# Optimization experiments

Measured on AMD Instinct MI355X. Metric: run time of the kernel, lower is better.

Reference implementation:

```python
import jax, jax.numpy as jnp
import numpy as np

IN_FEATURES = 4096
OUT_FEATURES = 768
N_BITS = 8
SCALE = float(2 ** N_BITS - 1)  # 255
REG_WEIGHT = 0.001


def setup_inputs() -> dict:
    key = jax.random.key(0)
    k1, k2, k3 = jax.random.split(key, 3)
    latent = jax.random.normal(k1, (1024, IN_FEATURES), dtype=jnp.float32)
    true_sum = jax.random.uniform(k2, (1024, OUT_FEATURES * N_BITS), dtype=jnp.float32)
    # nn.init.uniform_(weight, -0.1, 0.1)
    weight = jax.random.uniform(k3, (IN_FEATURES, OUT_FEATURES * N_BITS),
                                dtype=jnp.float32, minval=-0.1, maxval=0.1)
    return {"latent": latent, "true_sum": true_sum, "weight": weight}


def _powers():
    # [1, 2, 4, ..., 2^(n-1)] with the top (sign) bit negated -> two's complement
    p = 2.0 ** jnp.arange(N_BITS, dtype=jnp.float32)
    return p.at[-1].multiply(-1.0)


def reference(latent, true_sum, weight):
    prob_weights = jax.nn.sigmoid(weight)                      # [in, out*n_bits]
    # min(|p-0|, |p-1|) = min(p, 1-p) for p in (0,1)
    reg_loss = REG_WEIGHT * jnp.minimum(prob_weights, 1.0 - prob_weights).mean()

    powers = _powers()                                         # [n_bits]
    int_weights = jnp.einsum('iob,b->io',
                             prob_weights.reshape(IN_FEATURES, -1, N_BITS),
                             powers)                           # [in, out]
    int_sum = jnp.einsum('nob,b->no',
                         true_sum.reshape(true_sum.shape[0], -1, N_BITS),
                         powers)                               # [B, out]

    # (latent[:, :, None] * int_weights[None]).sum(-2) == latent @ int_weights
    pred = jnp.einsum('bi,io->bo', latent, int_weights)        # [B, out]

    recon_loss = jnp.mean((pred / SCALE - int_sum / SCALE) ** 2)
    return (recon_loss + reg_loss, recon_loss, reg_loss)
```

## Files before the change

### kernel.cpp

```cpp
#include <hip/hip_runtime.h>
#include <hip/hip_bf16.h>
#include <stdint.h>

#define IN_F   4096
#define OUT_F  768
#define OUTB   (OUT_F * 8)
#define BATCH  1024
#define SPLITK 4
#define KSPAN  (IN_F / SPLITK)
#define BK     64
#define NIT    (KSPAN / BK)
#define PLANE  (BATCH * OUT_F)
#define PLANE4 (PLANE / 4)
#define EPIBLK 768

#define WS_WP    12582912
#define WS_LABF  18874368
#define WS_REGP  27262976
#define WS_SQP   27269120

typedef short short8  __attribute__((ext_vector_type(8)));
typedef float f32x4   __attribute__((ext_vector_type(4)));
typedef unsigned int u32;

__device__ __forceinline__ ushort f2bf(float f) {
    uint32_t u = __builtin_bit_cast(uint32_t, f);
    u += 0x7FFFu + ((u >> 16) & 1u);
    return (ushort)(u >> 16);
}

__device__ __forceinline__ float waveReduceSum(float v) {
    #pragma unroll
    for (int off = 32; off > 0; off >>= 1) v += __shfl_down(v, off, 64);
    return v;
}

__device__ __forceinline__ void glds16(const void* g, void* l) {
    __builtin_amdgcn_global_load_lds(
        (const __attribute__((address_space(1))) u32*)g,
        (__attribute__((address_space(3))) u32*)l, 16, 0, 0);
}

__global__ __launch_bounds__(256) void k_weights(const float* __restrict__ w,
                                                 const float* __restrict__ latent,
                                                 ushort* __restrict__ wp,
                                                 ushort* __restrict__ labf,
                                                 float* __restrict__ regpart) {
    if (blockIdx.x >= 1536) {
        int t = (blockIdx.x - 1536) * 256 + threadIdx.x;
        const float4* src = (const float4*)latent;
        uint4* dst = (uint4*)labf;
        #pragma unroll
        for (int j = 0; j < 4; j++) {
            int o = j * 131072 + t;
            float4 a0 = src[2 * o];
            float4 a1 = src[2 * o + 1];
            union { ushort u[8]; uint4 v; } pk;
            pk.u[0] = f2bf(a0.x); pk.u[1] = f2bf(a0.y); pk.u[2] = f2bf(a0.z); pk.u[3] = f2bf(a0.w);
            pk.u[4] = f2bf(a1.x); pk.u[5] = f2bf(a1.y); pk.u[6] = f2bf(a1.z); pk.u[7] = f2bf(a1.w);
            dst[o] = pk.v;
        }
        return;
    }

    int t  = blockIdx.x * 256 + threadIdx.x;
    int o  = t % OUT_F;
    int i8 = t / OUT_F;
    const float* src = w + (size_t)(i8 * 8) * OUTB + (size_t)o * 8;

    const float P[8] = {1.f, 2.f, 4.f, 8.f, 16.f, 32.f, 64.f, -128.f};
    float regsum = 0.f;
    union { ushort u[8]; uint4 v; } pk;

    #pragma unroll
    for (int r = 0; r < 8; r++) {
        float4 a = *(const float4*)(src + (size_t)r * OUTB);
        float4 b = *(const float4*)(src + (size_t)r * OUTB + 4);
        float x[8] = {a.x, a.y, a.z, a.w, b.x, b.y, b.z, b.w};
        float iw = 0.f;
        #pragma unroll
        for (int j = 0; j < 8; j++) {
            float p = __builtin_amdgcn_rcpf(1.f + __expf(-x[j]));
            iw += p * P[j];
            regsum += fminf(p, 1.f - p);
        }
        pk.u[r] = f2bf(iw);
    }
    *(uint4*)(wp + ((size_t)i8 * OUT_F + o) * 8) = pk.v;

    float ws = waveReduceSum(regsum);
    __shared__ float red[4];
    int lane = threadIdx.x & 63, wv = threadIdx.x >> 6;
    if (lane == 0) red[wv] = ws;
    __syncthreads();
    if (threadIdx.x == 0) regpart[blockIdx.x] = red[0] + red[1] + red[2] + red[3];
}

__global__ __launch_bounds__(256) void k_gemm(const ushort* __restrict__ labf,
                                              const ushort* __restrict__ wp,
                                              float* __restrict__ predp) {
    __shared__ __align__(16) ushort lA3[3][64 * 64];
    __shared__ __align__(16) ushort lB3[3][8 * 512];

    const int tid  = threadIdx.x;
    const int n0   = blockIdx.x * 64;
    const int m0   = blockIdx.y * 64;
    const int bz   = blockIdx.z;
    const int kbase = bz * KSPAN;
    const int kg0   = kbase >> 3;
    const int lane = tid & 63, w = tid >> 6;
    const int wm = w >> 1, wn = w & 1;
    const int quad = lane >> 4, l16 = lane & 15;
    const int xA = (l16 & 7) << 4;

    f32x4 acc[2][2] = {{{0.f,0.f,0.f,0.f},{0.f,0.f,0.f,0.f}},
                       {{0.f,0.f,0.f,0.f},{0.f,0.f,0.f,0.f}}};

    const int r8 = lane >> 3;
    const int c8 = (lane & 7) ^ r8;
    const int p0 = 2 * w, p1 = 2 * w + 1;
    const ushort* aSrc0 = labf + (size_t)(m0 + 8 * p0 + r8) * IN_F + kbase + 8 * c8;
    const ushort* aSrc1 = labf + (size_t)(m0 + 8 * p1 + r8) * IN_F + kbase + 8 * c8;
    const ushort* bSrc0 = wp + ((size_t)(kg0 + p0) * OUT_F + n0 + lane) * 8;
    const ushort* bSrc1 = wp + ((size_t)(kg0 + p1) * OUT_F + n0 + lane) * 8;

    #define STAGE(bi, it_) do {                                                   \
        glds16(aSrc0 + (size_t)(it_) * BK,              &lA3[bi][p0 * 512]);      \
        glds16(aSrc1 + (size_t)(it_) * BK,              &lA3[bi][p1 * 512]);      \
        glds16(bSrc0 + (size_t)(it_) * (8 * OUT_F * 8), &lB3[bi][p0 * 512]);      \
        glds16(bSrc1 + (size_t)(it_) * (8 * OUT_F * 8), &lB3[bi][p1 * 512]);      \
    } while (0)

    #define MSTEP(bi) do {                                                        \
        const char* Ab = (const char*)&lA3[bi][0];                                \
        _Pragma("unroll")                                                         \
        for (int ss = 0; ss < 2; ++ss) {                                          \
            short8 af0 = *(const short8*)(Ab + ((wm * 32 + l16) << 7)             \
                                             + ((ss * 64 + quad * 16) ^ xA));     \
            short8 af1 = *(const short8*)(Ab + ((wm * 32 + 16 + l16) << 7)        \
                                             + ((ss * 64 + quad * 16) ^ xA));     \
            short8 bf0 = *(const short8*)&lB3[bi][(ss * 4 + quad) * 512           \
                                                  + (wn * 32 + l16) * 8];         \
            short8 bf1 = *(const short8*)&lB3[bi][(ss * 4 + quad) * 512           \
                                                  + (wn * 32 + 16 + l16) * 8];    \
            acc[0][0] = __builtin_amdgcn_mfma_f32_16x16x32_bf16(af0, bf0, acc[0][0], 0, 0, 0); \
            acc[0][1] = __builtin_amdgcn_mfma_f32_16x16x32_bf16(af0, bf1, acc[0][1], 0, 0, 0); \
            acc[1][0] = __builtin_amdgcn_mfma_f32_16x16x32_bf16(af1, bf0, acc[1][0], 0, 0, 0); \
            acc[1][1] = __builtin_amdgcn_mfma_f32_16x16x32_bf16(af1, bf1, acc[1][1], 0, 0, 0); \
        }                                                                         \
    } while (0)

    STAGE(0, 0);
    STAGE(1, 1);
    asm volatile("s_waitcnt vmcnt(4)" ::: "memory");
    __builtin_amdgcn_s_barrier();
    __builtin_amdgcn_sched_barrier(0);

    int bR = 0, bW = 2;
    for (int it = 0; it < NIT - 2; ++it) {
        STAGE(bW, it + 2);
        MSTEP(bR);
        asm volatile("s_waitcnt vmcnt(4)" ::: "memory");
        __builtin_amdgcn_s_barrier();
        __builtin_amdgcn_sched_barrier(0);
        bR = (bR + 1 == 3) ? 0 : bR + 1;
        bW = (bW + 1 == 3) ? 0 : bW + 1;
    }
    MSTEP(bR);
    asm volatile("s_waitcnt vmcnt(0)" ::: "memory");
    __builtin_amdgcn_s_barrier();
    __builtin_amdgcn_sched_barrier(0);
    bR = (bR + 1 == 3) ? 0 : bR + 1;
    MSTEP(bR);

    #undef STAGE
    #undef MSTEP

    float* plane = predp + (size_t)bz * PLANE;
    #pragma unroll
    for (int fm = 0; fm < 2; fm++)
    #pragma unroll
    for (int fn = 0; fn < 2; fn++)
    #pragma unroll
    for (int r = 0; r < 4; r++) {
        int m = m0 + wm * 32 + fm * 16 + quad * 4 + r;
        int n = n0 + wn * 32 + fn * 16 + l16;
        plane[(size_t)m * OUT_F + n] = acc[fm][fn][r];
    }
}

__global__ __launch_bounds__(256) void k_epi(const float* __restrict__ predp,
                                             const float* __restrict__ tsum,
                                             float* __restrict__ sqpart) {
    int g = blockIdx.x * 256 + threadIdx.x;
    int m = g / (OUT_F / 4);
    int c = g % (OUT_F / 4);
    const float4* pp = (const float4*)predp;
    float4 p0 = pp[g];
    float4 p1 = pp[g + PLANE4];
    float4 p2 = pp[g + 2 * PLANE4];
    float4 p3 = pp[g + 3 * PLANE4];
    float pv[4] = {p0.x + p1.x + p2.x + p3.x, p0.y + p1.y + p2.y + p3.y,
                   p0.z + p1.z + p2.z + p3.z, p0.w + p1.w + p2.w + p3.w};
    const float* ts = tsum + (size_t)m * OUTB + (size_t)c * 32;
    float lsum = 0.f;
    #pragma unroll
    for (int j = 0; j < 4; j++) {
        float4 t0 = *(const float4*)(ts + j * 8);
        float4 t1 = *(const float4*)(ts + j * 8 + 4);
        float isum = t0.x + 2.f * t0.y + 4.f * t0.z + 8.f * t0.w
                   + 16.f * t1.x + 32.f * t1.y + 64.f * t1.z - 128.f * t1.w;
        float d = pv[j] - isum;
        lsum += d * d;
    }
    float wsum = waveReduceSum(lsum);
    __shared__ float red[4];
    if ((threadIdx.x & 63) == 0) red[threadIdx.x >> 6] = wsum;
    __syncthreads();
    if (threadIdx.x == 0)
        sqpart[blockIdx.x] = red[0] + red[1] + red[2] + red[3];
}

__global__ __launch_bounds__(256) void k_fin(const float* __restrict__ regpart,
                                             const float* __restrict__ sqpart,
                                             float* __restrict__ out) {
    int tid = threadIdx.x;
    float r = 0.f, s = 0.f;
    #pragma unroll
    for (int j = 0; j < 6; j++) r += regpart[tid + j * 256];
    #pragma unroll
    for (int j = 0; j < 3; j++) s += sqpart[tid + j * 256];
    r = waveReduceSum(r);
    s = waveReduceSum(s);
    __shared__ float redR[4], redS[4];
    int lane = tid & 63, wv = tid >> 6;
    if (lane == 0) { redR[wv] = r; redS[wv] = s; }
    __syncthreads();
    if (tid == 0) {
        float R = redR[0] + redR[1] + redR[2] + redR[3];
        float S = redS[0] + redS[1] + redS[2] + redS[3];
        float recon = S / ((float)(BATCH * OUT_F) * 255.f * 255.f);
        float reg   = 0.001f * R / (float)((size_t)IN_F * OUTB);
        out[0] = recon + reg;
        out[1] = recon;
        out[2] = reg;
    }
}

extern "C" void kernel_launch(void* const* d_in, const int* in_sizes, int n_in,
                              void* d_out, int out_size, void* d_ws, size_t ws_size,
                              hipStream_t stream) {
    const float* latent = (const float*)d_in[0];
    const float* tsum   = (const float*)d_in[1];
    const float* weight = (const float*)d_in[2];
    float* out      = (float*)d_out;
    float* predp    = (float*)d_ws;
    ushort* wp      = (ushort*)((char*)d_ws + WS_WP);
    ushort* labf    = (ushort*)((char*)d_ws + WS_LABF);
    float* regpart  = (float*)((char*)d_ws + WS_REGP);
    float* sqpart   = (float*)((char*)d_ws + WS_SQP);

    k_weights<<<2048, 256, 0, stream>>>(weight, latent, wp, labf, regpart);
    k_gemm<<<dim3(OUT_F / 64, BATCH / 64, SPLITK), 256, 0, stream>>>(labf, wp, predp);
    k_epi<<<EPIBLK, 256, 0, stream>>>(predp, tsum, sqpart);
    k_fin<<<1, 256, 0, stream>>>(regpart, sqpart, out);
}
```

Measured before the change: 199.0 us.

## Enlarge GEMM tile to 128x192 with specialized loader waves and split-K 8

Rebuilds the GEMM around a 128x192 output tile per 384-thread block. Each wave now computes a 64x64 sub-tile with 16 MFMA accumulators, so more compute is done per byte loaded from LDS and global memory. Two waves load the A tile and four load the B tile, each waiting on its own outstanding-load count. The K step drops to 32 and split-K doubles to 8 to keep enough blocks in flight. The cost is that the partial-sum planes written and re-read by the epilogue double in size, and the workspace grows to match.

```diff
diff --git a/kernel.cpp b/kernel.cpp
--- a/kernel.cpp
+++ b/kernel.cpp
@@ -6,18 +6,20 @@
 #define OUT_F  768
 #define OUTB   (OUT_F * 8)
 #define BATCH  1024
-#define SPLITK 4
+#define SPLITK 8
 #define KSPAN  (IN_F / SPLITK)
-#define BK     64
-#define NIT    (KSPAN / BK)
+#define KSTEP  32
+#define NIT    (KSPAN / KSTEP)
+#define TN     192
+#define TM     128
 #define PLANE  (BATCH * OUT_F)
 #define PLANE4 (PLANE / 4)
 #define EPIBLK 768
 
-#define WS_WP    12582912
-#define WS_LABF  18874368
-#define WS_REGP  27262976
-#define WS_SQP   27269120
+#define WS_WP    25165824
+#define WS_LABF  31457280
+#define WS_REGP  39845888
+#define WS_SQP   39852032
 
 typedef short short8  __attribute__((ext_vector_type(8)));
 typedef float f32x4   __attribute__((ext_vector_type(4)));
@@ -96,63 +98,71 @@
     if (threadIdx.x == 0) regpart[blockIdx.x] = red[0] + red[1] + red[2] + red[3];
 }
 
-__global__ __launch_bounds__(256) void k_gemm(const ushort* __restrict__ labf,
+__global__ __launch_bounds__(384) void k_gemm(const ushort* __restrict__ labf,
                                               const ushort* __restrict__ wp,
                                               float* __restrict__ predp) {
-    __shared__ __align__(16) ushort lA3[3][64 * 64];
-    __shared__ __align__(16) ushort lB3[3][8 * 512];
+    __shared__ __align__(16) ushort lA[3][8 * 512];
+    __shared__ __align__(16) ushort lB[3][12 * 512];
 
     const int tid  = threadIdx.x;
-    const int n0   = blockIdx.x * 64;
-    const int m0   = blockIdx.y * 64;
+    const int lane = tid & 63, w = tid >> 6;
+    const int n0   = blockIdx.x * TN;
+    const int m0   = blockIdx.y * TM;
     const int bz   = blockIdx.z;
     const int kbase = bz * KSPAN;
     const int kg0   = kbase >> 3;
-    const int lane = tid & 63, w = tid >> 6;
-    const int wm = w >> 1, wn = w & 1;
     const int quad = lane >> 4, l16 = lane & 15;
-    const int xA = (l16 & 7) << 4;
-
-    f32x4 acc[2][2] = {{{0.f,0.f,0.f,0.f},{0.f,0.f,0.f,0.f}},
-                       {{0.f,0.f,0.f,0.f},{0.f,0.f,0.f,0.f}}};
-
-    const int r8 = lane >> 3;
-    const int c8 = (lane & 7) ^ r8;
-    const int p0 = 2 * w, p1 = 2 * w + 1;
-    const ushort* aSrc0 = labf + (size_t)(m0 + 8 * p0 + r8) * IN_F + kbase + 8 * c8;
-    const ushort* aSrc1 = labf + (size_t)(m0 + 8 * p1 + r8) * IN_F + kbase + 8 * c8;
-    const ushort* bSrc0 = wp + ((size_t)(kg0 + p0) * OUT_F + n0 + lane) * 8;
-    const ushort* bSrc1 = wp + ((size_t)(kg0 + p1) * OUT_F + n0 + lane) * 8;
-
-    #define STAGE(bi, it_) do {                                                   \
-        glds16(aSrc0 + (size_t)(it_) * BK,              &lA3[bi][p0 * 512]);      \
-        glds16(aSrc1 + (size_t)(it_) * BK,              &lA3[bi][p1 * 512]);      \
-        glds16(bSrc0 + (size_t)(it_) * (8 * OUT_F * 8), &lB3[bi][p0 * 512]);      \
-        glds16(bSrc1 + (size_t)(it_) * (8 * OUT_F * 8), &lB3[bi][p1 * 512]);      \
+    const int wmh = w & 1;
+    const int wnt = w >> 1;
+
+    f32x4 acc[4][4] = {};
+
+    const int r4 = lane >> 2, c4 = lane & 3;
+    const int kgw = w - 2;
+
+    #define STAGE(bi, it_) do {                                                        \
+        if (w < 2) {                                                                   \
+            _Pragma("unroll")                                                          \
+            for (int k = 0; k < 4; ++k) {                                              \
+                int p = 4 * w + k;                                                     \
+                glds16(labf + (size_t)(m0 + 16 * p + r4) * IN_F                        \
+                            + kbase + (it_) * KSTEP + c4 * 8,                          \
+                       &lA[bi][p * 512]);                                              \
+            }                                                                          \
+        } else {                                                                       \
+            _Pragma("unroll")                                                          \
+            for (int h = 0; h < 3; ++h) {                                              \
+                glds16(wp + ((size_t)(kg0 + (it_) * 4 + kgw) * OUT_F                   \
+                             + n0 + h * 64 + lane) * 8,                                \
+                       &lB[bi][(kgw * 3 + h) * 512]);                                  \
+            }                                                                          \
+        }                                                                              \
     } while (0)
 
-    #define MSTEP(bi) do {                                                        \
-        const char* Ab = (const char*)&lA3[bi][0];                                \
-        _Pragma("unroll")                                                         \
-        for (int ss = 0; ss < 2; ++ss) {                                          \
-            short8 af0 = *(const short8*)(Ab + ((wm * 32 + l16) << 7)             \
-                                             + ((ss * 64 + quad * 16) ^ xA));     \
-            short8 af1 = *(const short8*)(Ab + ((wm * 32 + 16 + l16) << 7)        \
-                                             + ((ss * 64 + quad * 16) ^ xA));     \
-            short8 bf0 = *(const short8*)&lB3[bi][(ss * 4 + quad) * 512           \
-                                                  + (wn * 32 + l16) * 8];         \
-            short8 bf1 = *(const short8*)&lB3[bi][(ss * 4 + quad) * 512           \
-                                                  + (wn * 32 + 16 + l16) * 8];    \
-            acc[0][0] = __builtin_amdgcn_mfma_f32_16x16x32_bf16(af0, bf0, acc[0][0], 0, 0, 0); \
-            acc[0][1] = __builtin_amdgcn_mfma_f32_16x16x32_bf16(af0, bf1, acc[0][1], 0, 0, 0); \
-            acc[1][0] = __builtin_amdgcn_mfma_f32_16x16x32_bf16(af1, bf0, acc[1][0], 0, 0, 0); \
-            acc[1][1] = __builtin_amdgcn_mfma_f32_16x16x32_bf16(af1, bf1, acc[1][1], 0, 0, 0); \
-        }                                                                         \
+    #define WAITOWN() do {                                                             \
+        if (w < 2) asm volatile("s_waitcnt vmcnt(4)" ::: "memory");                    \
+        else       asm volatile("s_waitcnt vmcnt(3)" ::: "memory");                    \
+    } while (0)
+
+    #define MSTEP(bi) do {                                                             \
+        short8 af[4], bf[4];                                                           \
+        _Pragma("unroll")                                                              \
+        for (int i = 0; i < 4; ++i)                                                    \
+            af[i] = *(const short8*)&lA[bi][(wmh * 64 + i * 16 + l16) * 32 + quad * 8];\
+        _Pragma("unroll")                                                              \
+        for (int j = 0; j < 4; ++j)                                                    \
+            bf[j] = *(const short8*)&lB[bi][(quad * 3 + wnt) * 512 + (j * 16 + l16) * 8];\
+        _Pragma("unroll")                                                              \
+        for (int i = 0; i < 4; ++i)                                                    \
+        _Pragma("unroll")                                                              \
+        for (int j = 0; j < 4; ++j)                                                    \
+            acc[i][j] = __builtin_amdgcn_mfma_f32_16x16x32_bf16(af[i], bf[j],          \
+                                                                acc[i][j], 0, 0, 0);   \
     } while (0)
 
     STAGE(0, 0);
     STAGE(1, 1);
-    asm volatile("s_waitcnt vmcnt(4)" ::: "memory");
+    WAITOWN();
     __builtin_amdgcn_s_barrier();
     __builtin_amdgcn_sched_barrier(0);
 
@@ -160,7 +170,7 @@
     for (int it = 0; it < NIT - 2; ++it) {
         STAGE(bW, it + 2);
         MSTEP(bR);
-        asm volatile("s_waitcnt vmcnt(4)" ::: "memory");
+        WAITOWN();
         __builtin_amdgcn_s_barrier();
         __builtin_amdgcn_sched_barrier(0);
         bR = (bR + 1 == 3) ? 0 : bR + 1;
@@ -174,18 +184,19 @@
     MSTEP(bR);
 
     #undef STAGE
+    #undef WAITOWN
     #undef MSTEP
 
     float* plane = predp + (size_t)bz * PLANE;
     #pragma unroll
-    for (int fm = 0; fm < 2; fm++)
-    #pragma unroll
-    for (int fn = 0; fn < 2; fn++)
+    for (int i = 0; i < 4; i++)
+    #pragma unroll
+    for (int j = 0; j < 4; j++)
     #pragma unroll
     for (int r = 0; r < 4; r++) {
-        int m = m0 + wm * 32 + fm * 16 + quad * 4 + r;
-        int n = n0 + wn * 32 + fn * 16 + l16;
-        plane[(size_t)m * OUT_F + n] = acc[fm][fn][r];
+        int m = m0 + wmh * 64 + i * 16 + quad * 4 + r;
+        int n = n0 + wnt * 64 + j * 16 + l16;
+        plane[(size_t)m * OUT_F + n] = acc[i][j][r];
     }
 }
 
@@ -196,12 +207,12 @@
     int m = g / (OUT_F / 4);
     int c = g % (OUT_F / 4);
     const float4* pp = (const float4*)predp;
-    float4 p0 = pp[g];
-    float4 p1 = pp[g + PLANE4];
-    float4 p2 = pp[g + 2 * PLANE4];
-    float4 p3 = pp[g + 3 * PLANE4];
-    float pv[4] = {p0.x + p1.x + p2.x + p3.x, p0.y + p1.y + p2.y + p3.y,
-                   p0.z + p1.z + p2.z + p3.z, p0.w + p1.w + p2.w + p3.w};
+    float pv[4] = {0.f, 0.f, 0.f, 0.f};
+    #pragma unroll
+    for (int p = 0; p < SPLITK; p++) {
+        float4 q = pp[g + p * PLANE4];
+        pv[0] += q.x; pv[1] += q.y; pv[2] += q.z; pv[3] += q.w;
+    }
     const float* ts = tsum + (size_t)m * OUTB + (size_t)c * 32;
     float lsum = 0.f;
     #pragma unroll
@@ -261,7 +272,7 @@
     float* sqpart   = (float*)((char*)d_ws + WS_SQP);
 
     k_weights<<<2048, 256, 0, stream>>>(weight, latent, wp, labf, regpart);
-    k_gemm<<<dim3(OUT_F / 64, BATCH / 64, SPLITK), 256, 0, stream>>>(labf, wp, predp);
+    k_gemm<<<dim3(OUT_F / TN, BATCH / TM, SPLITK), 384, 0, stream>>>(labf, wp, predp);
     k_epi<<<EPIBLK, 256, 0, stream>>>(predp, tsum, sqpart);
     k_fin<<<1, 256, 0, stream>>>(regpart, sqpart, out);
 }
```

Measured after the change: 197.8 us. No clear change (-0.6%).
